# Performance work log

Hardware: AMD Instinct MI355X
Metric: run time of the kernel (lower is better)

## Reference

```python
import math
import jax, jax.numpy as jnp
import numpy as np

B, T, N_FEAT, H = 16, 1024, 512, 8
D_K = N_FEAT // H  # 64


def setup_inputs() -> dict:
    key = jax.random.key(0)
    ks = jax.random.split(key, 16)
    s = 0.02
    return {
        "query": jax.random.normal(ks[0], (B, T, N_FEAT), jnp.float32),
        "key": jax.random.normal(ks[1], (B, T, N_FEAT), jnp.float32),
        "value": jax.random.normal(ks[2], (B, T, N_FEAT), jnp.float32),
        "pos_emb": jax.random.normal(ks[3], (1, T, N_FEAT), jnp.float32),
        "mask": jnp.zeros((B, 1, T), jnp.float32),  # additive bias, 0 = attend
        "Wq": jax.random.normal(ks[4], (N_FEAT, N_FEAT), jnp.float32) * s,
        "bq": jnp.zeros((N_FEAT,), jnp.float32),
        "Wk": jax.random.normal(ks[5], (N_FEAT, N_FEAT), jnp.float32) * s,
        "bk": jnp.zeros((N_FEAT,), jnp.float32),
        "Wv": jax.random.normal(ks[6], (N_FEAT, N_FEAT), jnp.float32) * s,
        "bv": jnp.zeros((N_FEAT,), jnp.float32),
        "Wo": jax.random.normal(ks[7], (N_FEAT, N_FEAT), jnp.float32) * s,
        "bo": jnp.zeros((N_FEAT,), jnp.float32),
        "Wpos": jax.random.normal(ks[8], (N_FEAT, N_FEAT), jnp.float32) * s,
        "pos_bias_u": jax.random.normal(ks[9], (H, D_K), jnp.float32) * 0.05,
        "pos_bias_v": jax.random.normal(ks[10], (H, D_K), jnp.float32) * 0.05,
    }


def reference(query, key, value, pos_emb, mask,
              Wq, bq, Wk, bk, Wv, bv, Wo, bo, Wpos,
              pos_bias_u, pos_bias_v):
    b, t, _ = query.shape
    h, d_k = pos_bias_u.shape
    # projections -> head-split
    q = (query @ Wq + bq).reshape(b, t, h, d_k)                 # (B,T,H,D)
    k = (key @ Wk + bk).reshape(b, -1, h, d_k).transpose(0, 2, 1, 3)    # (B,H,S,D)
    v = (value @ Wv + bv).reshape(b, -1, h, d_k).transpose(0, 2, 1, 3)  # (B,H,S,D)
    p = (pos_emb @ Wpos).reshape(pos_emb.shape[1], h, d_k).transpose(1, 0, 2)  # (H,S,D)
    # Transformer-XL content/position biased queries
    q_u = (q + pos_bias_u).transpose(0, 2, 1, 3)  # (B,H,T,D)
    q_v = (q + pos_bias_v).transpose(0, 2, 1, 3)  # (B,H,T,D)
    matrix_ac = jnp.einsum('bhtd,bhsd->bhts', q_u, k)
    matrix_bd = jnp.einsum('bhtd,hsd->bhts', q_v, p)
    scores = (matrix_ac + matrix_bd) / math.sqrt(d_k) + mask[:, None]  # (B,H,T,S)
    attn = jax.nn.softmax(scores, axis=-1)
    out = jnp.einsum('bhts,bhsd->bthd', attn, v).reshape(b, t, h * d_k)
    return out @ Wo + bo  # (B,T,n_feat)
```

## Files before the change

### kernel.cpp

```cpp
#include <hip/hip_runtime.h>

#define BB 16
#define TT 1024
#define HH 8
#define DD 64
#define NF 512

typedef __attribute__((ext_vector_type(4))) float f4;
typedef __attribute__((ext_vector_type(8))) short s8;
typedef __attribute__((ext_vector_type(2))) unsigned int u32x2;
typedef unsigned short u16;
typedef unsigned int u32;

#define LOG2E 1.4426950408889634f

__device__ __forceinline__ u16 f2bf(float x){
    unsigned int u = __builtin_bit_cast(unsigned int, x);
    u = (u + 0x7FFFu + ((u >> 16) & 1u)) >> 16;
    return (u16)u;
}
__device__ __forceinline__ float bf2f(u16 h){
    unsigned int u = ((unsigned int)h) << 16;
    return __builtin_bit_cast(float, u);
}
__device__ __forceinline__ u32 cvt_pk(float a, float b){
    u32 r; asm("v_cvt_pk_bf16_f32 %0, %1, %2" : "=v"(r) : "v"(a), "v"(b)); return r;
}
__device__ __forceinline__ float lo_bf(u32 p){ return __builtin_bit_cast(float, p << 16); }
__device__ __forceinline__ float hi_bf(u32 p){ return __builtin_bit_cast(float, p & 0xFFFF0000u); }

__global__ __launch_bounds__(256) void prep_w(const float* __restrict__ Wq,
    const float* __restrict__ Wk, const float* __restrict__ Wv,
    const float* __restrict__ Wpos, const float* __restrict__ Wo,
    u16* __restrict__ wtq, u16* __restrict__ wtk, u16* __restrict__ wtv,
    u16* __restrict__ wtp, u16* __restrict__ wohi, u16* __restrict__ wolo)
{
    __shared__ float tile[32][33];
    const int which = blockIdx.z;
    const float* W = which==0?Wq:which==1?Wk:which==2?Wv:which==3?Wpos:Wo;
    const int n0 = blockIdx.x*32, k0 = blockIdx.y*32;
    const int tc = threadIdx.x & 31, tr = threadIdx.x >> 5;
#pragma unroll
    for (int i=0;i<4;i++){ int r = tr + i*8; tile[r][tc] = W[(size_t)(k0+r)*NF + n0+tc]; }
    __syncthreads();
#pragma unroll
    for (int i=0;i<4;i++){
        int n = tr + i*8, k = tc;
        float val = tile[k][n];
        u16 hi = f2bf(val);
        size_t off = (size_t)(n0+n)*NF + k0+k;
        if (which==0) wtq[off]=hi; else if (which==1) wtk[off]=hi;
        else if (which==2) wtv[off]=hi; else if (which==3) wtp[off]=hi;
        else { wohi[off]=hi; wolo[off]=f2bf(val - bf2f(hi)); }
    }
}

template<int MODE>
__global__ __launch_bounds__(256) void gemm_bf16(const float* __restrict__ A,
                                                 const u16* __restrict__ Wt,
                                                 const float* __restrict__ bias,
                                                 const u16* __restrict__ padd,
                                                 u16* __restrict__ out)
{
    __shared__ __align__(16) u16 As[128*64];
    __shared__ __align__(16) u16 Bs[128*64];
    const int tid = threadIdx.x;
    const int row0 = blockIdx.x*128, col0 = blockIdx.y*128;
    const int wid = tid>>6, lane = tid&63, lm = lane&15, lg = lane>>4;
    const int wm = wid>>1, wn = wid&1;

    f4 acc[4][4];
#pragma unroll
    for (int i=0;i<4;i++)
#pragma unroll
        for (int j=0;j<4;j++) acc[i][j] = (f4){0.f,0.f,0.f,0.f};

    for (int k0=0;k0<NF;k0+=64){
        f4 areg[8]; s8 breg[4];
#pragma unroll
        for (int it=0; it<8; ++it){
            int idx = (it*256 + tid)*4;
            int m = idx>>6, k = idx&63;
            areg[it] = *(const f4*)(&A[(size_t)(row0+m)*NF + k0 + k]);
        }
#pragma unroll
        for (int it=0; it<4; ++it){
            int idx = (it*256 + tid)*8;
            int n = idx>>6, k = idx&63;
            breg[it] = *(const s8*)(&Wt[(size_t)(col0+n)*NF + k0 + k]);
        }
        __syncthreads();
#pragma unroll
        for (int it=0; it<8; ++it){
            int idx = (it*256+tid)*4;
            int m = idx>>6, k = idx&63;
            u32x2 pk;
            pk[0] = cvt_pk(areg[it][0], areg[it][1]);
            pk[1] = cvt_pk(areg[it][2], areg[it][3]);
            *(u32x2*)((char*)As + ((m*128 + k*2) ^ ((m&7)<<4))) = pk;
        }
#pragma unroll
        for (int it=0; it<4; ++it){
            int idx = (it*256+tid)*8;
            int n = idx>>6, k = idx&63;
            *(s8*)((char*)Bs + ((n*128 + k*2) ^ ((n&7)<<4))) = breg[it];
        }
        __syncthreads();
        s8 af[4][2], bf[4][2];
#pragma unroll
        for (int i=0;i<4;i++){
            int m = wm*64 + i*16 + lm;
#pragma unroll
            for (int c=0;c<2;c++)
                af[i][c] = *(const s8*)((char*)As + ((m*128 + c*64 + lg*16) ^ ((m&7)<<4)));
        }
#pragma unroll
        for (int j=0;j<4;j++){
            int n = wn*64 + j*16 + lm;
#pragma unroll
            for (int c=0;c<2;c++)
                bf[j][c] = *(const s8*)((char*)Bs + ((n*128 + c*64 + lg*16) ^ ((n&7)<<4)));
        }
#pragma unroll
        for (int i=0;i<4;i++)
#pragma unroll
            for (int j=0;j<4;j++)
#pragma unroll
                for (int c=0;c<2;c++)
                    acc[i][j] = __builtin_amdgcn_mfma_f32_16x16x32_bf16(af[i][c], bf[j][c], acc[i][j], 0,0,0);
    }

#pragma unroll
    for (int i=0;i<4;i++){
#pragma unroll
        for (int j=0;j<4;j++){
#pragma unroll
            for (int r=0;r<4;r++){
                const int m = row0 + wm*64 + i*16 + lg*4 + r;
                const int n = col0 + wn*64 + j*16 + lm;
                float val = acc[i][j][r];
                const int hh = n>>6, dd = n&63;
                if (MODE == 0){
                    out[(size_t)(hh*TT + m)*64 + dd] = f2bf(val);
                } else {
                    val += bias[n];
                    const int b_ = m>>10, t_ = m&1023;
                    if (MODE == 2) val += bf2f(padd[(size_t)(hh*TT + t_)*64 + dd]);
                    if (MODE == 3)
                        out[(((size_t)(b_*HH+hh))*DD + dd)*TT + t_] = f2bf(val);
                    else
                        out[((size_t)(b_*HH+hh)*TT + t_)*64 + dd] = f2bf(val);
                }
            }
        }
    }
}

__global__ __launch_bounds__(256) void gemm_final(const float* __restrict__ A,
    const u16* __restrict__ Bhg, const u16* __restrict__ Blg,
    const float* __restrict__ bias, float* __restrict__ out)
{
    __shared__ __align__(16) u16 Ah[128*64];
    __shared__ __align__(16) u16 Al[128*64];
    __shared__ __align__(16) u16 Bh[128*64];
    __shared__ __align__(16) u16 Bl[128*64];
    const int tid = threadIdx.x;
    const int row0 = blockIdx.x*128, col0 = blockIdx.y*128;
    const int wid = tid>>6, lane = tid&63, lm = lane&15, lg = lane>>4;
    const int wm = wid>>1, wn = wid&1;

    f4 acc[4][4];
#pragma unroll
    for (int i=0;i<4;i++)
#pragma unroll
        for (int j=0;j<4;j++) acc[i][j] = (f4){0.f,0.f,0.f,0.f};

    for (int k0=0;k0<NF;k0+=64){
        f4 areg[8]; s8 bhreg[4], blreg[4];
#pragma unroll
        for (int it=0; it<8; ++it){
            int idx = (it*256 + tid)*4;
            int m = idx>>6, k = idx&63;
            areg[it] = *(const f4*)(&A[(size_t)(row0+m)*NF + k0 + k]);
        }
#pragma unroll
        for (int it=0; it<4; ++it){
            int idx = (it*256 + tid)*8;
            int n = idx>>6, k = idx&63;
            bhreg[it] = *(const s8*)(&Bhg[(size_t)(col0+n)*NF + k0 + k]);
            blreg[it] = *(const s8*)(&Blg[(size_t)(col0+n)*NF + k0 + k]);
        }
        __syncthreads();
#pragma unroll
        for (int it=0; it<8; ++it){
            int idx = (it*256+tid)*4;
            int m = idx>>6, k = idx&63;
            u32 p0 = cvt_pk(areg[it][0], areg[it][1]);
            u32 p1 = cvt_pk(areg[it][2], areg[it][3]);
            u32 q0 = cvt_pk(areg[it][0]-lo_bf(p0), areg[it][1]-hi_bf(p0));
            u32 q1 = cvt_pk(areg[it][2]-lo_bf(p1), areg[it][3]-hi_bf(p1));
            int off = (m*128 + k*2) ^ ((m&7)<<4);
            *(u32x2*)((char*)Ah + off) = (u32x2){p0,p1};
            *(u32x2*)((char*)Al + off) = (u32x2){q0,q1};
        }
#pragma unroll
        for (int it=0; it<4; ++it){
            int idx = (it*256+tid)*8;
            int n = idx>>6, k = idx&63;
            int off = (n*128 + k*2) ^ ((n&7)<<4);
            *(s8*)((char*)Bh + off) = bhreg[it];
            *(s8*)((char*)Bl + off) = blreg[it];
        }
        __syncthreads();
#pragma unroll
        for (int c=0;c<2;c++){
            s8 ah[4], al[4], bh4[4], bl4[4];
#pragma unroll
            for (int i=0;i<4;i++){
                int m = wm*64 + i*16 + lm;
                int off = (m*128 + c*64 + lg*16) ^ ((m&7)<<4);
                ah[i] = *(const s8*)((char*)Ah + off);
                al[i] = *(const s8*)((char*)Al + off);
            }
#pragma unroll
            for (int j=0;j<4;j++){
                int n = wn*64 + j*16 + lm;
                int off = (n*128 + c*64 + lg*16) ^ ((n&7)<<4);
                bh4[j] = *(const s8*)((char*)Bh + off);
                bl4[j] = *(const s8*)((char*)Bl + off);
            }
#pragma unroll
            for (int i=0;i<4;i++)
#pragma unroll
                for (int j=0;j<4;j++){
                    acc[i][j] = __builtin_amdgcn_mfma_f32_16x16x32_bf16(al[i], bh4[j], acc[i][j], 0,0,0);
                    acc[i][j] = __builtin_amdgcn_mfma_f32_16x16x32_bf16(ah[i], bl4[j], acc[i][j], 0,0,0);
                    acc[i][j] = __builtin_amdgcn_mfma_f32_16x16x32_bf16(ah[i], bh4[j], acc[i][j], 0,0,0);
                }
        }
    }

#pragma unroll
    for (int i=0;i<4;i++)
#pragma unroll
        for (int j=0;j<4;j++)
#pragma unroll
            for (int r=0;r<4;r++){
                const int m = row0 + wm*64 + i*16 + lg*4 + r;
                const int n = col0 + wn*64 + j*16 + lm;
                out[(size_t)m*NF + n] = acc[i][j][r] + bias[n];
            }
}

__global__ __launch_bounds__(256) void sbias_kernel(const u16* __restrict__ kp,
                                                    const u16* __restrict__ p,
                                                    const float* __restrict__ pbu,
                                                    const float* __restrict__ pbv,
                                                    const float* __restrict__ mask,
                                                    float* __restrict__ sb)
{
    const int w    = blockIdx.x * 4 + (threadIdx.x >> 6);
    const int lane = threadIdx.x & 63;
    const int s = w & 1023;
    const int h = (w >> 10) & 7;
    const int b = w >> 13;
    const float u  = pbu[h * 64 + lane];
    const float wv = pbv[h * 64 + lane] - u;
    const float kv = bf2f(kp[((size_t)(b * HH + h) * TT + s) * 64 + lane]);
    const float pv = bf2f(p[(size_t)(h * TT + s) * 64 + lane]);
    float val = u * kv + wv * pv;
#pragma unroll
    for (int off = 32; off; off >>= 1) val += __shfl_xor(val, off);
    if (lane == 0)
        sb[(size_t)(b * HH + h) * TT + s] = (val * 0.125f + mask[b * TT + s]) * LOG2E;
}

#define ATTN_GLOAD(tile) do { \
  _Pragma("unroll") for (int it=0; it<2; ++it){ \
    int idx = (it*256+tid)*8; int row_ = idx>>6, col_ = idx&63; \
    kh[it] = *(const s8*)(kb + (size_t)((tile)*64+row_)*64 + col_); \
    vh[it] = *(const s8*)(vtb + (size_t)row_*TT + (tile)*64 + col_); } } while(0)

#define ATTN_SSTORE(buf) do { \
  _Pragma("unroll") for (int it=0; it<2; ++it){ \
    int idx = (it*256+tid)*8; int row_ = idx>>6, col_ = idx&63; \
    int off_ = (row_*128 + col_*2) ^ ((row_&7)<<4); \
    *(s8*)((char*)Ks[(buf)] + off_) = kh[it]; \
    *(s8*)((char*)Vt[(buf)] + off_) = vh[it]; } } while(0)

#define ATTN_QK(buf, scv) do { \
  _Pragma("unroll") for (int j=0;j<4;j++){ \
    int srow_ = j*16+lm; \
    s8 kf0 = *(const s8*)((char*)Ks[(buf)] + ((srow_*128 + lg*16) ^ ((srow_&7)<<4))); \
    s8 kf1 = *(const s8*)((char*)Ks[(buf)] + ((srow_*128 + 64 + lg*16) ^ ((srow_&7)<<4))); \
    scv[j] = __builtin_amdgcn_mfma_f32_16x16x32_bf16(kf0, qf[0], scv[j], 0,0,0); \
    scv[j] = __builtin_amdgcn_mfma_f32_16x16x32_bf16(kf1, qf[1], scv[j], 0,0,0); } } while(0)

__global__ __launch_bounds__(256,3) void attn7(const u16* __restrict__ q,
                                               const u16* __restrict__ kp,
                                               const u16* __restrict__ vt,
                                               const float* __restrict__ sb,
                                               float* __restrict__ ao)
{
    __shared__ __align__(16) u16 Ks[2][64*64];
    __shared__ __align__(16) u16 Vt[2][64*64];
    __shared__ __align__(16) u16 Ps[64*64];

    const int tid = threadIdx.x;
    const int wid = tid>>6, lane = tid&63, lm = lane&15, lg = lane>>4;
    const int bid = blockIdx.x;
    const int xcd = bid & 7, slot = bid >> 3;
    const int bh = xcd + 8*(slot >> 4);
    const int qt = slot & 15;
    const int t0 = qt*64;
    const int b = bh >> 3, h = bh & 7;
    const u16* qb  = q  + (size_t)bh*TT*64;
    const u16* kb  = kp + (size_t)bh*TT*64;
    const u16* vtb = vt + (size_t)bh*DD*TT;
    const float* sbb = sb + (size_t)bh*TT;

    s8 qf[2];
    qf[0] = *(const s8*)(qb + (size_t)(t0 + wid*16 + lm)*64 + lg*8);
    qf[1] = *(const s8*)(qb + (size_t)(t0 + wid*16 + lm)*64 + 32 + lg*8);

    f4 lsum4 = (f4){0.f,0.f,0.f,0.f};
    f4 oacc[4];
#pragma unroll
    for (int n=0;n<4;n++) oacc[n] = (f4){0.f,0.f,0.f,0.f};
    f4 sc_cur[4], sc_next[4];

    const float SCL = 0.125f * LOG2E;
    const int prow = wid*16 + lm;

    s8 kh[2], vh[2];

    ATTN_GLOAD(0);
    ATTN_SSTORE(0);
    ATTN_GLOAD(1);
    __syncthreads();
#pragma unroll
    for (int j=0;j<4;j++) sc_cur[j] = (f4){0.f,0.f,0.f,0.f};
    ATTN_QK(0, sc_cur);

    for (int i=0; i<16; ++i){
        const int cur = i & 1, nxt = cur ^ 1;

        if (i < 15) ATTN_SSTORE(nxt);
        if (i < 14) ATTN_GLOAD(i+2);
        __syncthreads();

        f4 sbf[4];
#pragma unroll
        for (int j=0;j<4;j++) sbf[j] = *(const f4*)(sbb + i*64 + 16*j + 4*lg);

        if (i < 15){
#pragma unroll
            for (int j=0;j<4;j++) sc_next[j] = (f4){0.f,0.f,0.f,0.f};
            __builtin_amdgcn_s_setprio(1);
            ATTN_QK(nxt, sc_next);
            __builtin_amdgcn_s_setprio(0);
        }

        s8 vtf[4][2];
#pragma unroll
        for (int n=0;n<4;n++){
            int drow = n*16 + lm;
#pragma unroll
            for (int c=0;c<2;c++)
                vtf[n][c] = *(const s8*)((char*)Vt[cur] + ((drow*128 + c*64 + lg*16) ^ ((drow&7)<<4)));
        }

        f4 p[4];
#pragma unroll
        for (int j=0;j<4;j++)
#pragma unroll
            for (int r=0;r<4;r++) p[j][r] = __builtin_exp2f(sc_cur[j][r]*SCL + sbf[j][r]);
        lsum4 += (p[0] + p[1]) + (p[2] + p[3]);

#pragma unroll
        for (int j=0;j<4;j++){
            u32x2 w;
            w[0] = cvt_pk(p[j][0], p[j][1]);
            w[1] = cvt_pk(p[j][2], p[j][3]);
            *(u32x2*)((char*)Ps + ((prow*128 + (16*j + 4*lg)*2) ^ ((prow&7)<<4))) = w;
        }
        s8 pf0 = *(const s8*)((char*)Ps + ((prow*128 +  0 + lg*16) ^ ((prow&7)<<4)));
        s8 pf1 = *(const s8*)((char*)Ps + ((prow*128 + 64 + lg*16) ^ ((prow&7)<<4)));

        __builtin_amdgcn_s_setprio(1);
#pragma unroll
        for (int n=0;n<4;n++){
            oacc[n] = __builtin_amdgcn_mfma_f32_16x16x32_bf16(vtf[n][0], pf0, oacc[n], 0,0,0);
            oacc[n] = __builtin_amdgcn_mfma_f32_16x16x32_bf16(vtf[n][1], pf1, oacc[n], 0,0,0);
        }
        __builtin_amdgcn_s_setprio(0);

        __syncthreads();
#pragma unroll
        for (int j=0;j<4;j++) sc_cur[j] = sc_next[j];
    }

    float ls = (lsum4[0]+lsum4[1]) + (lsum4[2]+lsum4[3]);
    ls += __shfl_xor(ls, 16);
    ls += __shfl_xor(ls, 32);
    const float inv = 1.f / ls;
    const size_t row = (size_t)(b*TT + t0 + wid*16 + lm)*NF + h*64;
#pragma unroll
    for (int n=0; n<4; ++n){
        f4 o = oacc[n] * inv;
        *(f4*)(&ao[row + n*16 + lg*4]) = o;
    }
}

extern "C" void kernel_launch(void* const* d_in, const int* in_sizes, int n_in,
                              void* d_out, int out_size, void* d_ws, size_t ws_size,
                              hipStream_t stream)
{
    const float* query   = (const float*)d_in[0];
    const float* key     = (const float*)d_in[1];
    const float* value   = (const float*)d_in[2];
    const float* pos_emb = (const float*)d_in[3];
    const float* mask    = (const float*)d_in[4];
    const float* Wq   = (const float*)d_in[5];
    const float* bq   = (const float*)d_in[6];
    const float* Wk   = (const float*)d_in[7];
    const float* bk   = (const float*)d_in[8];
    const float* Wv   = (const float*)d_in[9];
    const float* bv   = (const float*)d_in[10];
    const float* Wo   = (const float*)d_in[11];
    const float* bo   = (const float*)d_in[12];
    const float* Wpos = (const float*)d_in[13];
    const float* pbu  = (const float*)d_in[14];
    const float* pbv  = (const float*)d_in[15];
    float* out = (float*)d_out;

    char* ws = (char*)d_ws;
    size_t o = 0;
    u16* wtq  = (u16*)(ws + o); o += (size_t)NF*NF*2;
    u16* wtk  = (u16*)(ws + o); o += (size_t)NF*NF*2;
    u16* wtv  = (u16*)(ws + o); o += (size_t)NF*NF*2;
    u16* wtp  = (u16*)(ws + o); o += (size_t)NF*NF*2;
    u16* wohi = (u16*)(ws + o); o += (size_t)NF*NF*2;
    u16* wolo = (u16*)(ws + o); o += (size_t)NF*NF*2;
    u16* p_ws  = (u16*)(ws + o); o += (size_t)HH*TT*DD*2;
    u16* q_ws  = (u16*)(ws + o); o += (size_t)BB*HH*TT*DD*2;
    u16* kp_ws = (u16*)(ws + o); o += (size_t)BB*HH*TT*DD*2;
    u16* vt_ws = (u16*)(ws + o); o += (size_t)BB*HH*TT*DD*2;
    float* sb_ws = (float*)(ws + o); o += (size_t)BB*HH*TT*4;
    float* ao_ws = (float*)(ws + o); o += (size_t)BB*TT*NF*4;

    const dim3 blk(256);

    prep_w<<<dim3(16,16,5), blk, 0, stream>>>(Wq, Wk, Wv, Wpos, Wo,
                                              wtq, wtk, wtv, wtp, wohi, wolo);
    gemm_bf16<0><<<dim3(TT/128, 4), blk, 0, stream>>>(pos_emb, wtp, nullptr, nullptr, p_ws);
    gemm_bf16<1><<<dim3(BB*TT/128, 4), blk, 0, stream>>>(query, wtq, bq, nullptr, q_ws);
    gemm_bf16<2><<<dim3(BB*TT/128, 4), blk, 0, stream>>>(key,   wtk, bk, p_ws,    kp_ws);
    gemm_bf16<3><<<dim3(BB*TT/128, 4), blk, 0, stream>>>(value, wtv, bv, nullptr, vt_ws);
    sbias_kernel<<<dim3(BB*HH*TT/4), blk, 0, stream>>>(kp_ws, p_ws, pbu, pbv, mask, sb_ws);
    attn7<<<dim3(BB*HH*TT/64), blk, 0, stream>>>(q_ws, kp_ws, vt_ws, sb_ws, ao_ws);
    gemm_final<<<dim3(BB*TT/128, 4), blk, 0, stream>>>(ao_ws, wohi, wolo, bo, out);
}
```

Before: 196.9 us.

## Fold pos_bias_u into Q projection, shrink score-bias kernel, emit bf16 split attention output

pos_bias_u is added to Q inside the projection epilogue (new MODE 5). Because K already carries the positional term, the per-key bias then only needs (pbv - pbu)·p. That bias is computed once per head and position and broadcast across batches, so the bias kernel no longer reads the whole K tensor. The attention kernel now writes its output as bf16 hi/lo pairs, which removes the fp32-to-split conversion from the final GEMM. The attention loop is also unrolled by two to drop the score-register copy. The cost is a slightly different rounding path for q+u in bf16 and more code in the macro-expanded loop.

```diff
diff --git a/kernel.cpp b/kernel.cpp
--- a/kernel.cpp
+++ b/kernel.cpp
@@ -60,6 +60,7 @@
                                                  const u16* __restrict__ Wt,
                                                  const float* __restrict__ bias,
                                                  const u16* __restrict__ padd,
+                                                 const float* __restrict__ pbias,
                                                  u16* __restrict__ out)
 {
     __shared__ __align__(16) u16 As[128*64];
@@ -146,6 +147,7 @@
                     val += bias[n];
                     const int b_ = m>>10, t_ = m&1023;
                     if (MODE == 2) val += bf2f(padd[(size_t)(hh*TT + t_)*64 + dd]);
+                    if (MODE == 5) val += pbias[n];
                     if (MODE == 3)
                         out[(((size_t)(b_*HH+hh))*DD + dd)*TT + t_] = f2bf(val);
                     else
@@ -156,7 +158,8 @@
     }
 }
 
-__global__ __launch_bounds__(256) void gemm_final(const float* __restrict__ A,
+__global__ __launch_bounds__(256) void gemm_final(const u16* __restrict__ Ahg,
+    const u16* __restrict__ Alg,
     const u16* __restrict__ Bhg, const u16* __restrict__ Blg,
     const float* __restrict__ bias, float* __restrict__ out)
 {
@@ -176,38 +179,24 @@
         for (int j=0;j<4;j++) acc[i][j] = (f4){0.f,0.f,0.f,0.f};
 
     for (int k0=0;k0<NF;k0+=64){
-        f4 areg[8]; s8 bhreg[4], blreg[4];
-#pragma unroll
-        for (int it=0; it<8; ++it){
-            int idx = (it*256 + tid)*4;
-            int m = idx>>6, k = idx&63;
-            areg[it] = *(const f4*)(&A[(size_t)(row0+m)*NF + k0 + k]);
-        }
+        s8 ahreg[4], alreg[4], bhreg[4], blreg[4];
 #pragma unroll
         for (int it=0; it<4; ++it){
             int idx = (it*256 + tid)*8;
-            int n = idx>>6, k = idx&63;
-            bhreg[it] = *(const s8*)(&Bhg[(size_t)(col0+n)*NF + k0 + k]);
-            blreg[it] = *(const s8*)(&Blg[(size_t)(col0+n)*NF + k0 + k]);
+            int m = idx>>6, k = idx&63;
+            ahreg[it] = *(const s8*)(&Ahg[(size_t)(row0+m)*NF + k0 + k]);
+            alreg[it] = *(const s8*)(&Alg[(size_t)(row0+m)*NF + k0 + k]);
+            bhreg[it] = *(const s8*)(&Bhg[(size_t)(col0+m)*NF + k0 + k]);
+            blreg[it] = *(const s8*)(&Blg[(size_t)(col0+m)*NF + k0 + k]);
         }
         __syncthreads();
-#pragma unroll
-        for (int it=0; it<8; ++it){
-            int idx = (it*256+tid)*4;
-            int m = idx>>6, k = idx&63;
-            u32 p0 = cvt_pk(areg[it][0], areg[it][1]);
-            u32 p1 = cvt_pk(areg[it][2], areg[it][3]);
-            u32 q0 = cvt_pk(areg[it][0]-lo_bf(p0), areg[it][1]-hi_bf(p0));
-            u32 q1 = cvt_pk(areg[it][2]-lo_bf(p1), areg[it][3]-hi_bf(p1));
-            int off = (m*128 + k*2) ^ ((m&7)<<4);
-            *(u32x2*)((char*)Ah + off) = (u32x2){p0,p1};
-            *(u32x2*)((char*)Al + off) = (u32x2){q0,q1};
-        }
 #pragma unroll
         for (int it=0; it<4; ++it){
             int idx = (it*256+tid)*8;
-            int n = idx>>6, k = idx&63;
-            int off = (n*128 + k*2) ^ ((n&7)<<4);
+            int m = idx>>6, k = idx&63;
+            int off = (m*128 + k*2) ^ ((m&7)<<4);
+            *(s8*)((char*)Ah + off) = ahreg[it];
+            *(s8*)((char*)Al + off) = alreg[it];
             *(s8*)((char*)Bh + off) = bhreg[it];
             *(s8*)((char*)Bl + off) = blreg[it];
         }
@@ -252,27 +241,23 @@
             }
 }
 
-__global__ __launch_bounds__(256) void sbias_kernel(const u16* __restrict__ kp,
-                                                    const u16* __restrict__ p,
-                                                    const float* __restrict__ pbu,
-                                                    const float* __restrict__ pbv,
-                                                    const float* __restrict__ mask,
-                                                    float* __restrict__ sb)
+__global__ __launch_bounds__(256) void sbias2(const u16* __restrict__ p,
+                                              const float* __restrict__ pbu,
+                                              const float* __restrict__ pbv,
+                                              const float* __restrict__ mask,
+                                              float* __restrict__ sb)
 {
     const int w    = blockIdx.x * 4 + (threadIdx.x >> 6);
     const int lane = threadIdx.x & 63;
     const int s = w & 1023;
-    const int h = (w >> 10) & 7;
-    const int b = w >> 13;
-    const float u  = pbu[h * 64 + lane];
-    const float wv = pbv[h * 64 + lane] - u;
-    const float kv = bf2f(kp[((size_t)(b * HH + h) * TT + s) * 64 + lane]);
-    const float pv = bf2f(p[(size_t)(h * TT + s) * 64 + lane]);
-    float val = u * kv + wv * pv;
+    const int h = w >> 10;
+    const float diff = pbv[h*64 + lane] - pbu[h*64 + lane];
+    const float pv = bf2f(p[(size_t)(h*TT + s)*64 + lane]);
+    float val = diff * pv;
 #pragma unroll
     for (int off = 32; off; off >>= 1) val += __shfl_xor(val, off);
-    if (lane == 0)
-        sb[(size_t)(b * HH + h) * TT + s] = (val * 0.125f + mask[b * TT + s]) * LOG2E;
+    if (lane < BB)
+        sb[(size_t)(lane*HH + h)*TT + s] = (val * 0.125f + mask[lane*TT + s]) * LOG2E;
 }
 
 #define ATTN_GLOAD(tile) do { \
@@ -296,11 +281,52 @@
     scv[j] = __builtin_amdgcn_mfma_f32_16x16x32_bf16(kf0, qf[0], scv[j], 0,0,0); \
     scv[j] = __builtin_amdgcn_mfma_f32_16x16x32_bf16(kf1, qf[1], scv[j], 0,0,0); } } while(0)
 
-__global__ __launch_bounds__(256,3) void attn7(const u16* __restrict__ q,
+#define ATTN_STEP(i, CUR, SCUR, SNXT) do { \
+    if ((i) < 15) ATTN_SSTORE((CUR)^1); \
+    if ((i) < 14) ATTN_GLOAD((i)+2); \
+    __syncthreads(); \
+    f4 sbf[4]; \
+    _Pragma("unroll") for (int j=0;j<4;j++) sbf[j] = *(const f4*)(sbb + (i)*64 + 16*j + 4*lg); \
+    if ((i) < 15){ \
+        _Pragma("unroll") for (int j=0;j<4;j++) SNXT[j] = (f4){0.f,0.f,0.f,0.f}; \
+        __builtin_amdgcn_s_setprio(1); \
+        ATTN_QK((CUR)^1, SNXT); \
+        __builtin_amdgcn_s_setprio(0); \
+    } \
+    s8 vtf[4][2]; \
+    _Pragma("unroll") for (int n=0;n<4;n++){ \
+        int drow_ = n*16 + lm; \
+        _Pragma("unroll") for (int c=0;c<2;c++) \
+            vtf[n][c] = *(const s8*)((char*)Vt[(CUR)] + ((drow_*128 + c*64 + lg*16) ^ ((drow_&7)<<4))); \
+    } \
+    f4 p[4]; \
+    _Pragma("unroll") for (int j=0;j<4;j++) \
+        _Pragma("unroll") for (int r=0;r<4;r++) \
+            p[j][r] = __builtin_exp2f(SCUR[j][r]*SCL + sbf[j][r]); \
+    lsum4 += (p[0] + p[1]) + (p[2] + p[3]); \
+    _Pragma("unroll") for (int j=0;j<4;j++){ \
+        u32x2 w_; \
+        w_[0] = cvt_pk(p[j][0], p[j][1]); \
+        w_[1] = cvt_pk(p[j][2], p[j][3]); \
+        *(u32x2*)((char*)Ps + ((prow*128 + (16*j + 4*lg)*2) ^ ((prow&7)<<4))) = w_; \
+    } \
+    s8 pf0 = *(const s8*)((char*)Ps + ((prow*128 +  0 + lg*16) ^ ((prow&7)<<4))); \
+    s8 pf1 = *(const s8*)((char*)Ps + ((prow*128 + 64 + lg*16) ^ ((prow&7)<<4))); \
+    __builtin_amdgcn_s_setprio(1); \
+    _Pragma("unroll") for (int n=0;n<4;n++){ \
+        oacc[n] = __builtin_amdgcn_mfma_f32_16x16x32_bf16(vtf[n][0], pf0, oacc[n], 0,0,0); \
+        oacc[n] = __builtin_amdgcn_mfma_f32_16x16x32_bf16(vtf[n][1], pf1, oacc[n], 0,0,0); \
+    } \
+    __builtin_amdgcn_s_setprio(0); \
+    __syncthreads(); \
+} while(0)
+
+__global__ __launch_bounds__(256,3) void attn8(const u16* __restrict__ q,
                                                const u16* __restrict__ kp,
                                                const u16* __restrict__ vt,
                                                const float* __restrict__ sb,
-                                               float* __restrict__ ao)
+                                               u16* __restrict__ aoh,
+                                               u16* __restrict__ aol)
 {
     __shared__ __align__(16) u16 Ks[2][64*64];
     __shared__ __align__(16) u16 Vt[2][64*64];
@@ -327,7 +353,7 @@
     f4 oacc[4];
 #pragma unroll
     for (int n=0;n<4;n++) oacc[n] = (f4){0.f,0.f,0.f,0.f};
-    f4 sc_cur[4], sc_next[4];
+    f4 scA[4], scB[4];
 
     const float SCL = 0.125f * LOG2E;
     const int prow = wid*16 + lm;
@@ -339,65 +365,12 @@
     ATTN_GLOAD(1);
     __syncthreads();
 #pragma unroll
-    for (int j=0;j<4;j++) sc_cur[j] = (f4){0.f,0.f,0.f,0.f};
-    ATTN_QK(0, sc_cur);
-
-    for (int i=0; i<16; ++i){
-        const int cur = i & 1, nxt = cur ^ 1;
-
-        if (i < 15) ATTN_SSTORE(nxt);
-        if (i < 14) ATTN_GLOAD(i+2);
-        __syncthreads();
-
-        f4 sbf[4];
-#pragma unroll
-        for (int j=0;j<4;j++) sbf[j] = *(const f4*)(sbb + i*64 + 16*j + 4*lg);
-
-        if (i < 15){
-#pragma unroll
-            for (int j=0;j<4;j++) sc_next[j] = (f4){0.f,0.f,0.f,0.f};
-            __builtin_amdgcn_s_setprio(1);
-            ATTN_QK(nxt, sc_next);
-            __builtin_amdgcn_s_setprio(0);
-        }
-
-        s8 vtf[4][2];
-#pragma unroll
-        for (int n=0;n<4;n++){
-            int drow = n*16 + lm;
-#pragma unroll
-            for (int c=0;c<2;c++)
-                vtf[n][c] = *(const s8*)((char*)Vt[cur] + ((drow*128 + c*64 + lg*16) ^ ((drow&7)<<4)));
-        }
-
-        f4 p[4];
-#pragma unroll
-        for (int j=0;j<4;j++)
-#pragma unroll
-            for (int r=0;r<4;r++) p[j][r] = __builtin_exp2f(sc_cur[j][r]*SCL + sbf[j][r]);
-        lsum4 += (p[0] + p[1]) + (p[2] + p[3]);
-
-#pragma unroll
-        for (int j=0;j<4;j++){
-            u32x2 w;
-            w[0] = cvt_pk(p[j][0], p[j][1]);
-            w[1] = cvt_pk(p[j][2], p[j][3]);
-            *(u32x2*)((char*)Ps + ((prow*128 + (16*j + 4*lg)*2) ^ ((prow&7)<<4))) = w;
-        }
-        s8 pf0 = *(const s8*)((char*)Ps + ((prow*128 +  0 + lg*16) ^ ((prow&7)<<4)));
-        s8 pf1 = *(const s8*)((char*)Ps + ((prow*128 + 64 + lg*16) ^ ((prow&7)<<4)));
-
-        __builtin_amdgcn_s_setprio(1);
-#pragma unroll
-        for (int n=0;n<4;n++){
-            oacc[n] = __builtin_amdgcn_mfma_f32_16x16x32_bf16(vtf[n][0], pf0, oacc[n], 0,0,0);
-            oacc[n] = __builtin_amdgcn_mfma_f32_16x16x32_bf16(vtf[n][1], pf1, oacc[n], 0,0,0);
-        }
-        __builtin_amdgcn_s_setprio(0);
-
-        __syncthreads();
-#pragma unroll
-        for (int j=0;j<4;j++) sc_cur[j] = sc_next[j];
+    for (int j=0;j<4;j++) scA[j] = (f4){0.f,0.f,0.f,0.f};
+    ATTN_QK(0, scA);
+
+    for (int ii=0; ii<8; ++ii){
+        ATTN_STEP(2*ii,   0, scA, scB);
+        ATTN_STEP(2*ii+1, 1, scB, scA);
     }
 
     float ls = (lsum4[0]+lsum4[1]) + (lsum4[2]+lsum4[3]);
@@ -408,7 +381,12 @@
 #pragma unroll
     for (int n=0; n<4; ++n){
         f4 o = oacc[n] * inv;
-        *(f4*)(&ao[row + n*16 + lg*4]) = o;
+        u32 h0 = cvt_pk(o[0], o[1]);
+        u32 h1 = cvt_pk(o[2], o[3]);
+        u32 l0 = cvt_pk(o[0]-lo_bf(h0), o[1]-hi_bf(h0));
+        u32 l1 = cvt_pk(o[2]-lo_bf(h1), o[3]-hi_bf(h1));
+        *(u32x2*)(&aoh[row + n*16 + lg*4]) = (u32x2){h0,h1};
+        *(u32x2*)(&aol[row + n*16 + lg*4]) = (u32x2){l0,l1};
     }
 }
 
@@ -447,17 +425,18 @@
     u16* kp_ws = (u16*)(ws + o); o += (size_t)BB*HH*TT*DD*2;
     u16* vt_ws = (u16*)(ws + o); o += (size_t)BB*HH*TT*DD*2;
     float* sb_ws = (float*)(ws + o); o += (size_t)BB*HH*TT*4;
-    float* ao_ws = (float*)(ws + o); o += (size_t)BB*TT*NF*4;
+    u16* aoh_ws = (u16*)(ws + o); o += (size_t)BB*TT*NF*2;
+    u16* aol_ws = (u16*)(ws + o); o += (size_t)BB*TT*NF*2;
 
     const dim3 blk(256);
 
     prep_w<<<dim3(16,16,5), blk, 0, stream>>>(Wq, Wk, Wv, Wpos, Wo,
                                               wtq, wtk, wtv, wtp, wohi, wolo);
-    gemm_bf16<0><<<dim3(TT/128, 4), blk, 0, stream>>>(pos_emb, wtp, nullptr, nullptr, p_ws);
-    gemm_bf16<1><<<dim3(BB*TT/128, 4), blk, 0, stream>>>(query, wtq, bq, nullptr, q_ws);
-    gemm_bf16<2><<<dim3(BB*TT/128, 4), blk, 0, stream>>>(key,   wtk, bk, p_ws,    kp_ws);
-    gemm_bf16<3><<<dim3(BB*TT/128, 4), blk, 0, stream>>>(value, wtv, bv, nullptr, vt_ws);
-    sbias_kernel<<<dim3(BB*HH*TT/4), blk, 0, stream>>>(kp_ws, p_ws, pbu, pbv, mask, sb_ws);
-    attn7<<<dim3(BB*HH*TT/64), blk, 0, stream>>>(q_ws, kp_ws, vt_ws, sb_ws, ao_ws);
-    gemm_final<<<dim3(BB*TT/128, 4), blk, 0, stream>>>(ao_ws, wohi, wolo, bo, out);
-}
+    gemm_bf16<0><<<dim3(TT/128, 4), blk, 0, stream>>>(pos_emb, wtp, nullptr, nullptr, nullptr, p_ws);
+    sbias2<<<dim3(HH*TT/4), blk, 0, stream>>>(p_ws, pbu, pbv, mask, sb_ws);
+    gemm_bf16<5><<<dim3(BB*TT/128, 4), blk, 0, stream>>>(query, wtq, bq, nullptr, pbu, q_ws);
+    gemm_bf16<2><<<dim3(BB*TT/128, 4), blk, 0, stream>>>(key,   wtk, bk, p_ws, nullptr, kp_ws);
+    gemm_bf16<3><<<dim3(BB*TT/128, 4), blk, 0, stream>>>(value, wtv, bv, nullptr, nullptr, vt_ws);
+    attn8<<<dim3(BB*HH*TT/64), blk, 0, stream>>>(q_ws, kp_ws, vt_ws, sb_ws, aoh_ws, aol_ws);
+    gemm_final<<<dim3(BB*TT/128, 4), blk, 0, stream>>>(aoh_ws, aol_ws, wohi, wolo, bo, out);
+}
```

Result: faster. 179.4 us (median of 4 runs) (-8.9%).
